# Kernel optimization log

Hardware: AMD Instinct MI355X
Metric: run time of the kernel (lower is better)

The kernel has to match this reference:

```python
import jax, jax.numpy as jnp
import numpy as np

S, D, F = 4096, 1024, 4096
EPS = 1e-5

def _layernorm(x, g, b):
    mu = jnp.mean(x, axis=-1, keepdims=True)
    var = jnp.mean(jnp.square(x - mu), axis=-1, keepdims=True)
    return (x - mu) * jax.lax.rsqrt(var + EPS) * g + b

def setup_inputs() -> dict:
    key = jax.random.key(0)
    ks = jax.random.split(key, 16)
    s = 0.02
    inp = {
        "query": jax.random.normal(ks[0], (S, D), jnp.float32),
        "key":   jax.random.normal(ks[1], (S, D), jnp.float32),
        "value": jax.random.normal(ks[2], (S, D), jnp.float32),
        "mask":  jax.random.uniform(ks[3], (S, S), jnp.float32),
        # attention linears (stored [in, out]; y = x @ W + b)
        "Wq": jax.random.normal(ks[4], (D, D), jnp.float32) * s,
        "bq": jnp.zeros((D,), jnp.float32),
        "Wk": jax.random.normal(ks[5], (D, D), jnp.float32) * s,
        "bk": jnp.zeros((D,), jnp.float32),
        "Wv": jax.random.normal(ks[6], (D, D), jnp.float32) * s,
        "bv": jnp.zeros((D,), jnp.float32),
        "Wo": jax.random.normal(ks[7], (D, D), jnp.float32) * s,
        "bo": jnp.zeros((D,), jnp.float32),
        # layernorm 1
        "g1": jnp.ones((D,), jnp.float32),
        "be1": jnp.zeros((D,), jnp.float32),
        # feed forward
        "W1": jax.random.normal(ks[8], (D, F), jnp.float32) * s,
        "bf1": jnp.zeros((F,), jnp.float32),
        "W2": jax.random.normal(ks[9], (F, D), jnp.float32) * s,
        "bf2": jnp.zeros((D,), jnp.float32),
        # layernorm 2
        "g2": jnp.ones((D,), jnp.float32),
        "be2": jnp.zeros((D,), jnp.float32),
    }
    return inp

def reference(query, key, value, mask, Wq, bq, Wk, bk, Wv, bv, Wo, bo,
              g1, be1, W1, bf1, W2, bf2, g2, be2):
    q = query @ Wq + bq                      # [S, D]
    k = key @ Wk + bk                        # [S, D]
    v = value @ Wv + bv                      # [S, D]
    scores = q @ k.T                         # [S, S]
    masked = scores * mask                   # multiplicative mask
    h = jax.nn.softmax(masked / jnp.sqrt(jnp.float32(D)), axis=0)  # softmax over dim 0
    attn = (h @ v) @ Wo + bo                 # [S, D]
    # dropout is identity in eval mode
    n1 = _layernorm(attn + query, g1, be1)
    ff = jax.nn.relu(n1 @ W1 + bf1) @ W2 + bf2
    return _layernorm(ff + n1, g2, be2)
```

## Files before the change

kernel.cpp:

```cpp
#include <hip/hip_runtime.h>
#include <hip/hip_bf16.h>

#define S_DIM 4096
#define D_DIM 1024
#define F_DIM 4096

typedef unsigned short ushort_t;
typedef __attribute__((ext_vector_type(8))) short sh8;
typedef __attribute__((ext_vector_type(4))) short sh4;
typedef __attribute__((ext_vector_type(4))) float fx4;

__device__ __forceinline__ ushort_t f2bf(float f) {
    union { float f; unsigned u; } v; v.f = f;
    unsigned r = v.u + 0x7fffu + ((v.u >> 16) & 1u);
    return (ushort_t)(r >> 16);
}
__device__ __forceinline__ float bf2f(ushort_t u) {
    union { unsigned u; float f; } v; v.u = ((unsigned)u) << 16;
    return v.f;
}

typedef const __attribute__((address_space(1))) void* gvp;
typedef __attribute__((address_space(3))) void* svp;
__device__ __forceinline__ void gload_lds16(const void* g, void* l) {
    __builtin_amdgcn_global_load_lds((gvp)g, (svp)l, 16, 0, 0);
}

#define BM 128
#define BN 128
#define BK 32
#define LDS_BUF 16384

template<bool BIAS, bool RELU, bool SCALE, bool OUTBF, bool SPLITK>
__device__ __forceinline__
void gemm_body(const ushort_t* A, const ushort_t* Bt,
               const float* bias,
               float* Cf, ushort_t* Cb,
               int M, int N, int K, int kBeg, int kEnd, float scale)
{
    __shared__ ushort_t lds[3 * (BM * BK + BN * BK)];
    const int tid = threadIdx.x;
    const int bm = blockIdx.x, bn = blockIdx.y;
    const int w  = tid >> 6, l = tid & 63;
    const int wm = w >> 1, wn = w & 1;

    fx4 acc[4][4] = {};

    const ushort_t* Ag = A  + (size_t)(bm * BM) * K;
    const ushort_t* Bg = Bt + (size_t)(bn * BN) * K;

    const int srow = tid >> 2;
    const int scs  = (tid & 3) ^ (srow & 3);

    auto stage = [&](int b, int k0) {
        char* base = (char*)lds + b * LDS_BUF;
        #pragma unroll
        for (int c = 0; c < 2; ++c) {
            int row = c * 64 + srow;
            gload_lds16(Ag + (size_t)row * K + k0 + scs * 8,
                        base + c * 4096 + tid * 16);
            gload_lds16(Bg + (size_t)row * K + k0 + scs * 8,
                        base + 8192 + c * 4096 + tid * 16);
        }
    };

    const int nt = (kEnd - kBeg) / BK;

    stage(0, kBeg);
    if (nt > 1) {
        stage(1, kBeg + BK);
        asm volatile("s_waitcnt vmcnt(4)" ::: "memory");
    } else {
        asm volatile("s_waitcnt vmcnt(0)" ::: "memory");
    }
    __builtin_amdgcn_s_barrier();
    __builtin_amdgcn_sched_barrier(0);

    int cur = 0;
    for (int t = 0; t < nt; ++t) {
        int stg = cur + 2; if (stg >= 3) stg -= 3;
        if (t + 2 < nt) stage(stg, kBeg + (t + 2) * BK);

        char* lbase = (char*)lds + cur * LDS_BUF;
        sh8 af[4], bfr[4];
        #pragma unroll
        for (int q = 0; q < 4; ++q) {
            int ra = wm * 64 + q * 16 + (l & 15);
            int ca = (l >> 4) ^ (ra & 3);
            af[q]  = *(const sh8*)(lbase + ra * 64 + ca * 16);
            int rb = wn * 64 + q * 16 + (l & 15);
            int cb = (l >> 4) ^ (rb & 3);
            bfr[q] = *(const sh8*)(lbase + 8192 + rb * 64 + cb * 16);
        }
        #pragma unroll
        for (int i = 0; i < 4; ++i)
            #pragma unroll
            for (int j = 0; j < 4; ++j)
                acc[i][j] = __builtin_amdgcn_mfma_f32_16x16x32_bf16(
                                af[i], bfr[j], acc[i][j], 0, 0, 0);

        asm volatile("s_waitcnt lgkmcnt(0)" ::: "memory");
        if (t + 2 < nt)      asm volatile("s_waitcnt vmcnt(4)" ::: "memory");
        else if (t + 1 < nt) asm volatile("s_waitcnt vmcnt(0)" ::: "memory");
        if (t + 1 < nt) {
            __builtin_amdgcn_s_barrier();
            __builtin_amdgcn_sched_barrier(0);
        }
        cur = cur + 1; if (cur == 3) cur = 0;
    }

    if (SPLITK) Cb += (size_t)blockIdx.z * M * N;

    const int crow0 = bm * BM + wm * 64;
    const int ccol0 = bn * BN + wn * 64;
    #pragma unroll
    for (int i = 0; i < 4; ++i) {
        #pragma unroll
        for (int j = 0; j < 4; ++j) {
            int col = ccol0 + j * 16 + (l & 15);
            float bia = BIAS ? bias[col] : 0.f;
            #pragma unroll
            for (int r = 0; r < 4; ++r) {
                int row = crow0 + i * 16 + (l >> 4) * 4 + r;
                float v = acc[i][j][r] + bia;
                if (SCALE) v *= scale;
                if (RELU) v = fmaxf(v, 0.f);
                if (OUTBF) Cb[(size_t)row * N + col] = f2bf(v);
                else       Cf[(size_t)row * N + col] = v;
            }
        }
    }
}

template<bool BIAS, bool RELU, bool SCALE, bool OUTBF>
__global__ __launch_bounds__(256)
void gemm_bt(const ushort_t* __restrict__ A, const ushort_t* __restrict__ Bt,
             const float* __restrict__ bias,
             float* __restrict__ Cf, ushort_t* __restrict__ Cb,
             int M, int N, int K, float scale)
{
    gemm_body<BIAS, RELU, SCALE, OUTBF, false>(A, Bt, bias, Cf, Cb,
                                               M, N, K, 0, K, scale);
}

__global__ __launch_bounds__(256)
void gemm_bt_sk(const ushort_t* __restrict__ A, const ushort_t* __restrict__ Bt,
                ushort_t* __restrict__ Cpart, int M, int N, int K, int Ks)
{
    int z = blockIdx.z;
    gemm_body<false, false, false, true, true>(A, Bt, nullptr,
                                               nullptr, Cpart,
                                               M, N, K, z * Ks, z * Ks + Ks, 1.f);
}

__global__ __launch_bounds__(256)
void qkv_gemm(const ushort_t* qin, const ushort_t* kin, const ushort_t* vin,
              const ushort_t* WqT, const ushort_t* WkT, const ushort_t* WvT,
              const float* bq, const float* bk, const float* bv,
              ushort_t* qb, ushort_t* kb, ushort_t* vb, int M, int N, int K)
{
    const ushort_t* A; const ushort_t* Bt; const float* bias; ushort_t* C;
    if (blockIdx.z == 0)      { A = qin; Bt = WqT; bias = bq; C = qb; }
    else if (blockIdx.z == 1) { A = kin; Bt = WkT; bias = bk; C = kb; }
    else                      { A = vin; Bt = WvT; bias = bv; C = vb; }
    gemm_body<true, false, false, true, false>(A, Bt, bias,
                                               nullptr, C, M, N, K, 0, K, 1.f);
}

#define G2_BM 256
#define G2_BN 256
#define G2_BUF 32768

template<bool BIAS, bool RELU, bool SCALE, bool OUTBF, bool SPLITK>
__device__ __forceinline__
void gemm256_body(const ushort_t* A, const ushort_t* Bt,
                  const float* bias,
                  float* Cf, ushort_t* Cb,
                  int M, int N, int K, int kBeg, int kEnd, float scale)
{
    __shared__ ushort_t lds[3 * (G2_BM * BK + G2_BN * BK)];
    const int tid = threadIdx.x;
    const int bm = blockIdx.x, bn = blockIdx.y;
    const int w  = tid >> 6, l = tid & 63;
    const int wm = w >> 2, wn = w & 3;

    fx4 acc[8][4] = {};

    const ushort_t* Ag = A  + (size_t)(bm * G2_BM) * K;
    const ushort_t* Bg = Bt + (size_t)(bn * G2_BN) * K;

    auto stage = [&](int b, int k0) {
        char* base = (char*)lds + b * G2_BUF;
        #pragma unroll
        for (int c = 0; c < 2; ++c) {
            int idx = c * 512 + tid;
            int row = idx >> 2;
            int cs  = idx & 3;
            gload_lds16(Ag + (size_t)row * K + k0 + cs * 8,
                        base + idx * 16);
            gload_lds16(Bg + (size_t)row * K + k0 + cs * 8,
                        base + 16384 + idx * 16);
        }
    };

    const int nt = (kEnd - kBeg) / BK;

    stage(0, kBeg);
    if (nt > 1) {
        stage(1, kBeg + BK);
        asm volatile("s_waitcnt vmcnt(4)" ::: "memory");
    } else {
        asm volatile("s_waitcnt vmcnt(0)" ::: "memory");
    }
    __builtin_amdgcn_s_barrier();
    __builtin_amdgcn_sched_barrier(0);

    int cur = 0;
    for (int t = 0; t < nt; ++t) {
        int stg = cur + 2; if (stg >= 3) stg -= 3;
        if (t + 2 < nt) stage(stg, kBeg + (t + 2) * BK);

        char* lbase = (char*)lds + cur * G2_BUF;
        sh8 af[8], bfr[4];
        #pragma unroll
        for (int q = 0; q < 8; ++q) {
            int ra = wm * 128 + q * 16 + (l & 15);
            af[q] = *(const sh8*)(lbase + ra * 64 + (l >> 4) * 16);
        }
        #pragma unroll
        for (int j = 0; j < 4; ++j) {
            int rb = wn * 64 + j * 16 + (l & 15);
            bfr[j] = *(const sh8*)(lbase + 16384 + rb * 64 + (l >> 4) * 16);
        }
        #pragma unroll
        for (int i = 0; i < 8; ++i)
            #pragma unroll
            for (int j = 0; j < 4; ++j)
                acc[i][j] = __builtin_amdgcn_mfma_f32_16x16x32_bf16(
                                af[i], bfr[j], acc[i][j], 0, 0, 0);

        asm volatile("s_waitcnt lgkmcnt(0)" ::: "memory");
        if (t + 2 < nt)      asm volatile("s_waitcnt vmcnt(4)" ::: "memory");
        else if (t + 1 < nt) asm volatile("s_waitcnt vmcnt(0)" ::: "memory");
        if (t + 1 < nt) {
            __builtin_amdgcn_s_barrier();
            __builtin_amdgcn_sched_barrier(0);
        }
        cur = cur + 1; if (cur == 3) cur = 0;
    }

    if (SPLITK) Cb += (size_t)blockIdx.z * M * N;

    const int crow0 = bm * G2_BM + wm * 128;
    const int ccol0 = bn * G2_BN + wn * 64;
    #pragma unroll
    for (int i = 0; i < 8; ++i) {
        #pragma unroll
        for (int j = 0; j < 4; ++j) {
            int col = ccol0 + j * 16 + (l & 15);
            float bia = BIAS ? bias[col] : 0.f;
            #pragma unroll
            for (int r = 0; r < 4; ++r) {
                int row = crow0 + i * 16 + (l >> 4) * 4 + r;
                float v = acc[i][j][r] + bia;
                if (SCALE) v *= scale;
                if (RELU) v = fmaxf(v, 0.f);
                if (OUTBF) Cb[(size_t)row * N + col] = f2bf(v);
                else       Cf[(size_t)row * N + col] = v;
            }
        }
    }
}

template<bool BIAS, bool RELU, bool SCALE, bool OUTBF>
__global__ __launch_bounds__(512)
void gemm256_bt(const ushort_t* __restrict__ A, const ushort_t* __restrict__ Bt,
                const float* __restrict__ bias,
                float* __restrict__ Cf, ushort_t* __restrict__ Cb,
                int M, int N, int K, float scale)
{
    gemm256_body<BIAS, RELU, SCALE, OUTBF, false>(A, Bt, bias, Cf, Cb,
                                                  M, N, K, 0, K, scale);
}

__global__ __launch_bounds__(512)
void gemm256_bt_sk(const ushort_t* __restrict__ A, const ushort_t* __restrict__ Bt,
                   ushort_t* __restrict__ Cpart, int M, int N, int K, int Ks)
{
    int z = blockIdx.z;
    gemm256_body<false, false, false, true, true>(A, Bt, nullptr,
                                                  nullptr, Cpart,
                                                  M, N, K, z * Ks, z * Ks + Ks, 1.f);
}

template<int NS>
__global__ __launch_bounds__(256)
void reduce_sk(const ushort_t* __restrict__ parts, ushort_t* __restrict__ ob,
               size_t MN)
{
    size_t idx = ((size_t)blockIdx.x * 256 + threadIdx.x) * 8;
    float s[8] = {0.f, 0.f, 0.f, 0.f, 0.f, 0.f, 0.f, 0.f};
    #pragma unroll
    for (int p = 0; p < NS; ++p) {
        sh8 v = *(const sh8*)(parts + (size_t)p * MN + idx);
        #pragma unroll
        for (int j = 0; j < 8; ++j) s[j] += bf2f((ushort_t)v[j]);
    }
    sh8 r;
    #pragma unroll
    for (int j = 0; j < 8; ++j) r[j] = (short)f2bf(s[j]);
    *(sh8*)(ob + idx) = r;
}

__global__ __launch_bounds__(256)
void transpose_f32_bf16(const float* __restrict__ in, ushort_t* __restrict__ out,
                        int R, int C)
{
    __shared__ float t[32][33];
    int bc = blockIdx.x * 32, br = blockIdx.y * 32;
    int tx = threadIdx.x & 31, ty = threadIdx.x >> 5;
    #pragma unroll
    for (int i = 0; i < 32; i += 8)
        t[ty + i][tx] = in[(size_t)(br + ty + i) * C + bc + tx];
    __syncthreads();
    #pragma unroll
    for (int i = 0; i < 32; i += 8)
        out[(size_t)(bc + ty + i) * R + br + tx] = f2bf(t[tx][ty + i]);
}

__global__ __launch_bounds__(256)
void transpose4_f32_bf16(const float* w0, const float* w1,
                         const float* w2, const float* w3,
                         ushort_t* o0, ushort_t* o1, ushort_t* o2, ushort_t* o3)
{
    const int R = D_DIM, C = D_DIM;
    const float* in; ushort_t* out;
    if (blockIdx.z == 0)      { in = w0; out = o0; }
    else if (blockIdx.z == 1) { in = w1; out = o1; }
    else if (blockIdx.z == 2) { in = w2; out = o2; }
    else                      { in = w3; out = o3; }
    __shared__ float t[32][33];
    int bc = blockIdx.x * 32, br = blockIdx.y * 32;
    int tx = threadIdx.x & 31, ty = threadIdx.x >> 5;
    #pragma unroll
    for (int i = 0; i < 32; i += 8)
        t[ty + i][tx] = in[(size_t)(br + ty + i) * C + bc + tx];
    __syncthreads();
    #pragma unroll
    for (int i = 0; i < 32; i += 8)
        out[(size_t)(bc + ty + i) * R + br + tx] = f2bf(t[tx][ty + i]);
}

__global__ __launch_bounds__(256)
void transpose_bf16(const ushort_t* __restrict__ in, ushort_t* __restrict__ out,
                    int R, int C)
{
    __shared__ ushort_t t[32][33];
    int bc = blockIdx.x * 32, br = blockIdx.y * 32;
    int tx = threadIdx.x & 31, ty = threadIdx.x >> 5;
    #pragma unroll
    for (int i = 0; i < 32; i += 8)
        t[ty + i][tx] = in[(size_t)(br + ty + i) * C + bc + tx];
    __syncthreads();
    #pragma unroll
    for (int i = 0; i < 32; i += 8)
        out[(size_t)(bc + ty + i) * R + br + tx] = t[tx][ty + i];
}

__global__ __launch_bounds__(256)
void cvt_bf16_3(const float* a, const float* b, const float* c,
                ushort_t* oa, ushort_t* ob, ushort_t* oc)
{
    const float* in; ushort_t* out;
    if (blockIdx.y == 0)      { in = a; out = oa; }
    else if (blockIdx.y == 1) { in = b; out = ob; }
    else                      { in = c; out = oc; }
    int i = (blockIdx.x * 256 + threadIdx.x) * 8;
    const float4* p = (const float4*)(in + i);
    float4 x = p[0], y = p[1];
    sh8 r;
    r[0] = (short)f2bf(x.x); r[1] = (short)f2bf(x.y);
    r[2] = (short)f2bf(x.z); r[3] = (short)f2bf(x.w);
    r[4] = (short)f2bf(y.x); r[5] = (short)f2bf(y.y);
    r[6] = (short)f2bf(y.z); r[7] = (short)f2bf(y.w);
    *(sh8*)(out + i) = r;
}

#define NCH 256
#define ROWS_PER_CH (S_DIM / NCH)

__global__ __launch_bounds__(256)
void smax_pass1(ushort_t* __restrict__ m, const float* __restrict__ mask,
                float* __restrict__ pmax, float* __restrict__ psum)
{
    int c0 = (blockIdx.x * 256 + threadIdx.x) * 8;
    int chunk = blockIdx.y;
    int r0 = chunk * ROWS_PER_CH;

    float mx[8], sm[8];
    #pragma unroll
    for (int j = 0; j < 8; ++j) { mx[j] = -1e30f; sm[j] = 0.f; }

    for (int i = 0; i < ROWS_PER_CH; ++i) {
        size_t off = (size_t)(r0 + i) * S_DIM + c0;
        sh8 mv = *(const sh8*)(m + off);
        float4 k0 = ((const float4*)(mask + off))[0];
        float4 k1 = ((const float4*)(mask + off))[1];
        float mk[8] = {k0.x, k0.y, k0.z, k0.w, k1.x, k1.y, k1.z, k1.w};
        sh8 wv;
        #pragma unroll
        for (int j = 0; j < 8; ++j) {
            float v0 = bf2f((ushort_t)mv[j]) * mk[j];
            ushort_t wb = f2bf(v0);
            wv[j] = (short)wb;
            float v = bf2f(wb);
            float nm = fmaxf(mx[j], v);
            sm[j] = sm[j] * __expf(mx[j] - nm) + __expf(v - nm);
            mx[j] = nm;
        }
        *(sh8*)(m + off) = wv;
    }
    #pragma unroll
    for (int j = 0; j < 8; ++j) {
        pmax[(size_t)(c0 + j) * NCH + chunk] = mx[j];
        psum[(size_t)(c0 + j) * NCH + chunk] = sm[j];
    }
}

__global__ __launch_bounds__(256)
void smax_pass2(const float* __restrict__ pmax, const float* __restrict__ psum,
                float* __restrict__ cmax, float* __restrict__ cinv)
{
    int col = blockIdx.x, t = threadIdx.x;
    float m = pmax[(size_t)col * NCH + t];
    float s = psum[(size_t)col * NCH + t];

    __shared__ float red[8];
    int w = t >> 6, l = t & 63;

    float mx = m;
    #pragma unroll
    for (int off = 32; off; off >>= 1) mx = fmaxf(mx, __shfl_down(mx, off));
    if (!l) red[w] = mx;
    __syncthreads();
    mx = fmaxf(fmaxf(red[0], red[1]), fmaxf(red[2], red[3]));
    __syncthreads();

    float sc = s * __expf(m - mx);
    #pragma unroll
    for (int off = 32; off; off >>= 1) sc += __shfl_down(sc, off);
    if (!l) red[4 + w] = sc;
    __syncthreads();
    if (t == 0) {
        float total = red[4] + red[5] + red[6] + red[7];
        cmax[col] = mx;
        cinv[col] = 1.f / total;
    }
}

__global__ __launch_bounds__(256)
void smax_pass3(const ushort_t* __restrict__ m,
                const float* __restrict__ cmax, const float* __restrict__ cinv,
                ushort_t* __restrict__ h)
{
    size_t idx = ((size_t)blockIdx.x * 256 + threadIdx.x) * 8;
    int col0 = (int)(idx & (S_DIM - 1));
    sh8 mv = *(const sh8*)(m + idx);
    sh8 r;
    #pragma unroll
    for (int j = 0; j < 8; ++j) {
        int c = col0 + j;
        float v = bf2f((ushort_t)mv[j]);
        r[j] = (short)f2bf(__expf(v - cmax[c]) * cinv[c]);
    }
    *(sh8*)(h + idx) = r;
}

template<int NS, bool WB>
__global__ __launch_bounds__(256)
void add_ln_sk(const ushort_t* __restrict__ parts, const float* __restrict__ pbias,
               const float* __restrict__ resid, const float* __restrict__ g,
               const float* __restrict__ be,
               float* __restrict__ of, ushort_t* __restrict__ ob)
{
    const int D = D_DIM;
    const size_t SD = (size_t)S_DIM * D_DIM;
    int row = blockIdx.x, tid = threadIdx.x;
    size_t base = (size_t)row * D + tid * 4;

    float4 vr = *(const float4*)(resid + base);
    float4 vbi = ((const float4*)pbias)[tid];
    float x0 = vr.x + vbi.x, x1 = vr.y + vbi.y, x2 = vr.z + vbi.z, x3 = vr.w + vbi.w;
    #pragma unroll
    for (int p = 0; p < NS; ++p) {
        sh4 v = *(const sh4*)(parts + p * SD + base);
        x0 += bf2f((ushort_t)v[0]); x1 += bf2f((ushort_t)v[1]);
        x2 += bf2f((ushort_t)v[2]); x3 += bf2f((ushort_t)v[3]);
    }

    float s = x0 + x1 + x2 + x3;
    float q = x0 * x0 + x1 * x1 + x2 * x2 + x3 * x3;
    #pragma unroll
    for (int off = 32; off; off >>= 1) {
        s += __shfl_down(s, off);
        q += __shfl_down(q, off);
    }
    __shared__ float red[8];
    int w = tid >> 6, l = tid & 63;
    if (!l) { red[w] = s; red[4 + w] = q; }
    __syncthreads();
    s = red[0] + red[1] + red[2] + red[3];
    q = red[4] + red[5] + red[6] + red[7];
    float mu = s * (1.f / D);
    float rstd = rsqrtf(q * (1.f / D) - mu * mu + 1e-5f);
    float4 vg  = ((const float4*)g)[tid];
    float4 vbe = ((const float4*)be)[tid];
    float y0 = (x0 - mu) * rstd * vg.x + vbe.x;
    float y1 = (x1 - mu) * rstd * vg.y + vbe.y;
    float y2 = (x2 - mu) * rstd * vg.z + vbe.z;
    float y3 = (x3 - mu) * rstd * vg.w + vbe.w;
    float4 r; r.x = y0; r.y = y1; r.z = y2; r.w = y3;
    *(float4*)(of + base) = r;
    if (WB) {
        sh4 rb;
        rb[0] = (short)f2bf(y0); rb[1] = (short)f2bf(y1);
        rb[2] = (short)f2bf(y2); rb[3] = (short)f2bf(y3);
        *(sh4*)(ob + base) = rb;
    }
}

extern "C" void kernel_launch(void* const* d_in, const int* in_sizes, int n_in,
                              void* d_out, int out_size, void* d_ws, size_t ws_size,
                              hipStream_t stream)
{
    const float* query = (const float*)d_in[0];
    const float* key_  = (const float*)d_in[1];
    const float* value = (const float*)d_in[2];
    const float* mask  = (const float*)d_in[3];
    const float* Wq = (const float*)d_in[4];  const float* bq = (const float*)d_in[5];
    const float* Wk = (const float*)d_in[6];  const float* bk = (const float*)d_in[7];
    const float* Wv = (const float*)d_in[8];  const float* bv = (const float*)d_in[9];
    const float* Wo = (const float*)d_in[10]; const float* bo = (const float*)d_in[11];
    const float* g1 = (const float*)d_in[12]; const float* be1 = (const float*)d_in[13];
    const float* W1 = (const float*)d_in[14]; const float* bf1 = (const float*)d_in[15];
    const float* W2 = (const float*)d_in[16]; const float* bf2 = (const float*)d_in[17];
    const float* g2 = (const float*)d_in[18]; const float* be2 = (const float*)d_in[19];

    const size_t MB = 1ull << 20;
    char* ws = (char*)d_ws;
    ushort_t* WqT = (ushort_t*)(ws);
    ushort_t* WkT = (ushort_t*)(ws + 2 * MB);
    ushort_t* WvT = (ushort_t*)(ws + 4 * MB);
    ushort_t* WoT = (ushort_t*)(ws + 6 * MB);
    ushort_t* W1T = (ushort_t*)(ws + 8 * MB);
    ushort_t* W2T = (ushort_t*)(ws + 16 * MB);
    ushort_t* qin = (ushort_t*)(ws + 24 * MB);
    ushort_t* kin = (ushort_t*)(ws + 32 * MB);
    ushort_t* vin = (ushort_t*)(ws + 40 * MB);
    ushort_t* qb  = (ushort_t*)(ws + 48 * MB);
    ushort_t* kb  = (ushort_t*)(ws + 56 * MB);
    ushort_t* vb  = (ushort_t*)(ws + 64 * MB);
    ushort_t* vT  = (ushort_t*)(ws + 72 * MB);
    ushort_t* msc = (ushort_t*)(ws + 80 * MB);
    ushort_t* hb  = (ushort_t*)(ws + 112 * MB);
    float*   pmax = (float*)(ws + 144 * MB);
    float*   psum = (float*)(ws + 148 * MB);
    float*   cmax = (float*)(ws + 152 * MB);
    float*   cinv = (float*)(ws + 152 * MB + 64 * 1024);
    ushort_t* pts1  = (ushort_t*)(ws + 80 * MB);
    ushort_t* apb   = (ushort_t*)(ws + 24 * MB);
    ushort_t* pts2  = (ushort_t*)(ws + 80 * MB);
    float*    n1f   = (float*)(ws + 48 * MB);
    ushort_t* n1b   = (ushort_t*)(ws + 64 * MB);
    ushort_t* mid   = (ushort_t*)(ws + 112 * MB);
    ushort_t* pts3  = (ushort_t*)(ws + 80 * MB);

    const int S = S_DIM, D = D_DIM, F = F_DIM;

    transpose4_f32_bf16<<<dim3(D / 32, D / 32, 4), 256, 0, stream>>>(
        Wq, Wk, Wv, Wo, WqT, WkT, WvT, WoT);
    transpose_f32_bf16<<<dim3(F / 32, D / 32), 256, 0, stream>>>(W1, W1T, D, F);
    transpose_f32_bf16<<<dim3(D / 32, F / 32), 256, 0, stream>>>(W2, W2T, F, D);

    cvt_bf16_3<<<dim3(S * D / 8 / 256, 3), 256, 0, stream>>>(
        query, key_, value, qin, kin, vin);

    qkv_gemm<<<dim3(S / BM, D / BN, 3), 256, 0, stream>>>(
        qin, kin, vin, WqT, WkT, WvT, bq, bk, bv, qb, kb, vb, S, D, D);

    transpose_bf16<<<dim3(D / 32, S / 32), 256, 0, stream>>>(vb, vT, S, D);

    gemm256_bt<false, false, true, true><<<dim3(S / G2_BM, S / G2_BN), 512, 0, stream>>>(
        qb, kb, nullptr, nullptr, msc, S, S, D, 0.03125f);

    smax_pass1<<<dim3(S / 2048, NCH), 256, 0, stream>>>(msc, mask, pmax, psum);
    smax_pass2<<<S, 256, 0, stream>>>(pmax, psum, cmax, cinv);
    smax_pass3<<<(size_t)S * S / 8 / 256, 256, 0, stream>>>(msc, cmax, cinv, hb);

    gemm256_bt_sk<<<dim3(S / G2_BM, D / G2_BN, 4), 512, 0, stream>>>(
        hb, vT, pts1, S, D, S, S / 4);
    reduce_sk<4><<<S * D / 2048, 256, 0, stream>>>(pts1, apb, (size_t)S * D);

    gemm_bt_sk<<<dim3(S / BM, D / BN, 2), 256, 0, stream>>>(apb, WoT, pts2, S, D, D, D / 2);

    add_ln_sk<2, true><<<S, 256, 0, stream>>>(pts2, bo, query, g1, be1, n1f, n1b);

    gemm256_bt<true, true, false, true><<<dim3(S / G2_BM, F / G2_BN), 512, 0, stream>>>(
        n1b, W1T, bf1, nullptr, mid, S, F, D, 1.f);

    gemm256_bt_sk<<<dim3(S / G2_BM, D / G2_BN, 4), 512, 0, stream>>>(
        mid, W2T, pts3, S, D, F, F / 4);

    add_ln_sk<4, false><<<S, 256, 0, stream>>>(pts3, bf2, n1f, g2, be2,
                                               (float*)d_out, nullptr);
}
```

Measured before the change: 335.7 us.

## Fuse mask multiply into score GEMM, swizzle blocks across XCDs, rework softmax reductions

The multiplicative mask is now applied in the score GEMM epilogue, so softmax pass 1 no longer reads the fp32 mask or rewrites the bf16 score matrix. Pass 1 partials are stored column-contiguous, and pass 2 becomes one thread per column with a serial online merge instead of a block-wide reduction. All GEMMs also remap block indices so that neighbouring tiles land on the same XCD, aiming for better L2 reuse. The epilogue's mask loads are strided per lane and may be poorly coalesced. The swizzle assumes the block count divides evenly by 8.

```diff
diff --git a/kernel.cpp b/kernel.cpp
--- a/kernel.cpp
+++ b/kernel.cpp
@@ -24,6 +24,16 @@
 typedef __attribute__((address_space(3))) void* svp;
 __device__ __forceinline__ void gload_lds16(const void* g, void* l) {
     __builtin_amdgcn_global_load_lds((gvp)g, (svp)l, 16, 0, 0);
+}
+
+__device__ __forceinline__ void xcd_swz(int& bm, int& bn) {
+    int gx = gridDim.x;
+    int n  = gx * gridDim.y;
+    int wg = blockIdx.y * gx + blockIdx.x;
+    int q  = n >> 3;
+    int sw = (wg & 7) * q + (wg >> 3);
+    bm = sw % gx;
+    bn = sw / gx;
 }
 
 #define BM 128
@@ -40,7 +50,7 @@
 {
     __shared__ ushort_t lds[3 * (BM * BK + BN * BK)];
     const int tid = threadIdx.x;
-    const int bm = blockIdx.x, bn = blockIdx.y;
+    int bm, bn; xcd_swz(bm, bn);
     const int w  = tid >> 6, l = tid & 63;
     const int wm = w >> 1, wn = w & 1;
 
@@ -171,16 +181,16 @@
 #define G2_BN 256
 #define G2_BUF 32768
 
-template<bool BIAS, bool RELU, bool SCALE, bool OUTBF, bool SPLITK>
+template<bool BIAS, bool RELU, bool SCALE, bool MASKMUL, bool OUTBF, bool SPLITK>
 __device__ __forceinline__
 void gemm256_body(const ushort_t* A, const ushort_t* Bt,
-                  const float* bias,
+                  const float* bias, const float* mask,
                   float* Cf, ushort_t* Cb,
                   int M, int N, int K, int kBeg, int kEnd, float scale)
 {
     __shared__ ushort_t lds[3 * (G2_BM * BK + G2_BN * BK)];
     const int tid = threadIdx.x;
-    const int bm = blockIdx.x, bn = blockIdx.y;
+    int bm, bn; xcd_swz(bm, bn);
     const int w  = tid >> 6, l = tid & 63;
     const int wm = w >> 2, wn = w & 3;
 
@@ -264,6 +274,7 @@
                 int row = crow0 + i * 16 + (l >> 4) * 4 + r;
                 float v = acc[i][j][r] + bia;
                 if (SCALE) v *= scale;
+                if (MASKMUL) v *= mask[(size_t)row * N + col];
                 if (RELU) v = fmaxf(v, 0.f);
                 if (OUTBF) Cb[(size_t)row * N + col] = f2bf(v);
                 else       Cf[(size_t)row * N + col] = v;
@@ -272,15 +283,15 @@
     }
 }
 
-template<bool BIAS, bool RELU, bool SCALE, bool OUTBF>
+template<bool BIAS, bool RELU, bool SCALE, bool MASKMUL, bool OUTBF>
 __global__ __launch_bounds__(512)
 void gemm256_bt(const ushort_t* __restrict__ A, const ushort_t* __restrict__ Bt,
-                const float* __restrict__ bias,
+                const float* __restrict__ bias, const float* __restrict__ mask,
                 float* __restrict__ Cf, ushort_t* __restrict__ Cb,
                 int M, int N, int K, float scale)
 {
-    gemm256_body<BIAS, RELU, SCALE, OUTBF, false>(A, Bt, bias, Cf, Cb,
-                                                  M, N, K, 0, K, scale);
+    gemm256_body<BIAS, RELU, SCALE, MASKMUL, OUTBF, false>(
+        A, Bt, bias, mask, Cf, Cb, M, N, K, 0, K, scale);
 }
 
 __global__ __launch_bounds__(512)
@@ -288,9 +299,9 @@
                    ushort_t* __restrict__ Cpart, int M, int N, int K, int Ks)
 {
     int z = blockIdx.z;
-    gemm256_body<false, false, false, true, true>(A, Bt, nullptr,
-                                                  nullptr, Cpart,
-                                                  M, N, K, z * Ks, z * Ks + Ks, 1.f);
+    gemm256_body<false, false, false, false, true, true>(
+        A, Bt, nullptr, nullptr, nullptr, Cpart,
+        M, N, K, z * Ks, z * Ks + Ks, 1.f);
 }
 
 template<int NS>
@@ -390,7 +401,7 @@
 #define ROWS_PER_CH (S_DIM / NCH)
 
 __global__ __launch_bounds__(256)
-void smax_pass1(ushort_t* __restrict__ m, const float* __restrict__ mask,
+void smax_pass1(const ushort_t* __restrict__ m,
                 float* __restrict__ pmax, float* __restrict__ psum)
 {
     int c0 = (blockIdx.x * 256 + threadIdx.x) * 8;
@@ -404,26 +415,18 @@
     for (int i = 0; i < ROWS_PER_CH; ++i) {
         size_t off = (size_t)(r0 + i) * S_DIM + c0;
         sh8 mv = *(const sh8*)(m + off);
-        float4 k0 = ((const float4*)(mask + off))[0];
-        float4 k1 = ((const float4*)(mask + off))[1];
-        float mk[8] = {k0.x, k0.y, k0.z, k0.w, k1.x, k1.y, k1.z, k1.w};
-        sh8 wv;
         #pragma unroll
         for (int j = 0; j < 8; ++j) {
-            float v0 = bf2f((ushort_t)mv[j]) * mk[j];
-            ushort_t wb = f2bf(v0);
-            wv[j] = (short)wb;
-            float v = bf2f(wb);
+            float v = bf2f((ushort_t)mv[j]);
             float nm = fmaxf(mx[j], v);
             sm[j] = sm[j] * __expf(mx[j] - nm) + __expf(v - nm);
             mx[j] = nm;
         }
-        *(sh8*)(m + off) = wv;
     }
     #pragma unroll
     for (int j = 0; j < 8; ++j) {
-        pmax[(size_t)(c0 + j) * NCH + chunk] = mx[j];
-        psum[(size_t)(c0 + j) * NCH + chunk] = sm[j];
+        pmax[(size_t)chunk * S_DIM + c0 + j] = mx[j];
+        psum[(size_t)chunk * S_DIM + c0 + j] = sm[j];
     }
 }
 
@@ -431,31 +434,17 @@
 void smax_pass2(const float* __restrict__ pmax, const float* __restrict__ psum,
                 float* __restrict__ cmax, float* __restrict__ cinv)
 {
-    int col = blockIdx.x, t = threadIdx.x;
-    float m = pmax[(size_t)col * NCH + t];
-    float s = psum[(size_t)col * NCH + t];
-
-    __shared__ float red[8];
-    int w = t >> 6, l = t & 63;
-
-    float mx = m;
-    #pragma unroll
-    for (int off = 32; off; off >>= 1) mx = fmaxf(mx, __shfl_down(mx, off));
-    if (!l) red[w] = mx;
-    __syncthreads();
-    mx = fmaxf(fmaxf(red[0], red[1]), fmaxf(red[2], red[3]));
-    __syncthreads();
-
-    float sc = s * __expf(m - mx);
-    #pragma unroll
-    for (int off = 32; off; off >>= 1) sc += __shfl_down(sc, off);
-    if (!l) red[4 + w] = sc;
-    __syncthreads();
-    if (t == 0) {
-        float total = red[4] + red[5] + red[6] + red[7];
-        cmax[col] = mx;
-        cinv[col] = 1.f / total;
-    }
+    int col = blockIdx.x * 256 + threadIdx.x;
+    float mx = -1e30f, sm = 0.f;
+    for (int c = 0; c < NCH; ++c) {
+        float m2 = pmax[(size_t)c * S_DIM + col];
+        float s2 = psum[(size_t)c * S_DIM + col];
+        float nm = fmaxf(mx, m2);
+        sm = sm * __expf(mx - nm) + s2 * __expf(m2 - nm);
+        mx = nm;
+    }
+    cmax[col] = mx;
+    cinv[col] = 1.f / sm;
 }
 
 __global__ __launch_bounds__(256)
@@ -590,11 +579,12 @@
 
     transpose_bf16<<<dim3(D / 32, S / 32), 256, 0, stream>>>(vb, vT, S, D);
 
-    gemm256_bt<false, false, true, true><<<dim3(S / G2_BM, S / G2_BN), 512, 0, stream>>>(
-        qb, kb, nullptr, nullptr, msc, S, S, D, 0.03125f);
-
-    smax_pass1<<<dim3(S / 2048, NCH), 256, 0, stream>>>(msc, mask, pmax, psum);
-    smax_pass2<<<S, 256, 0, stream>>>(pmax, psum, cmax, cinv);
+    gemm256_bt<false, false, true, true, true>
+        <<<dim3(S / G2_BM, S / G2_BN), 512, 0, stream>>>(
+        qb, kb, nullptr, mask, nullptr, msc, S, S, D, 0.03125f);
+
+    smax_pass1<<<dim3(S / 2048, NCH), 256, 0, stream>>>(msc, pmax, psum);
+    smax_pass2<<<S / 256, 256, 0, stream>>>(pmax, psum, cmax, cinv);
     smax_pass3<<<(size_t)S * S / 8 / 256, 256, 0, stream>>>(msc, cmax, cinv, hb);
 
     gemm256_bt_sk<<<dim3(S / G2_BM, D / G2_BN, 4), 512, 0, stream>>>(
@@ -605,8 +595,9 @@
 
     add_ln_sk<2, true><<<S, 256, 0, stream>>>(pts2, bo, query, g1, be1, n1f, n1b);
 
-    gemm256_bt<true, true, false, true><<<dim3(S / G2_BM, F / G2_BN), 512, 0, stream>>>(
-        n1b, W1T, bf1, nullptr, mid, S, F, D, 1.f);
+    gemm256_bt<true, true, false, false, true>
+        <<<dim3(S / G2_BM, F / G2_BN), 512, 0, stream>>>(
+        n1b, W1T, bf1, nullptr, nullptr, mid, S, F, D, 1.f);
 
     gemm256_bt_sk<<<dim3(S / G2_BM, D / G2_BN, 4), 512, 0, stream>>>(
         mid, W2T, pts3, S, D, F, F / 4);
```

Result: slower. 346.0 us (+3.1%).
